# Kernel optimization log

Measured on AMD Instinct MI355X. Metric: run time of the kernel, lower is better.

## Reference

```python
import jax, jax.numpy as jnp
import numpy as np

TAU = 0.2  # temperature from __init__
EPS = 1e-12  # F.normalize eps


def setup_inputs() -> dict:
    key = jax.random.key(0)
    k1, k2, k3 = jax.random.split(key, 3)
    N, D = 131072, 1024
    return {
        "query": jax.random.normal(k1, (D,), dtype=jnp.float32),
        "K": jax.random.normal(k2, (N, D), dtype=jnp.float32),
        "V": jax.random.normal(k3, (N, D), dtype=jnp.float32),
        "topk": 32,
    }


def reference(query, K, V, topk):
    # q = F.normalize(query, dim=-1)
    q = query / jnp.maximum(jnp.linalg.norm(query, axis=-1, keepdims=True), EPS)
    # logits: [N] cosine-sim / tau (K rows are assumed pre-normalized by write())
    logits = (K @ q) / TAU
    # top-k branch (N > topk)
    vals, idxs = jax.lax.top_k(logits, topk)          # [topk], [topk]
    attn = jax.nn.softmax(vals, axis=-1)              # [topk]
    out = attn @ V[idxs]                              # [D]
    full_attn = jnp.zeros_like(logits).at[idxs].set(attn)  # [N]
    return out, full_attn
```

## Files before the change

### kernel.cpp

```cpp
#include <hip/hip_runtime.h>
#include <float.h>
#include <math.h>

#define DIM    1024
#define NROWS  131072
#define TOPK   32
#define TAU    0.2f
#define CHUNK  512
#define NCHUNK (NROWS / CHUNK)
#define NCAND  (NCHUNK * TOPK)

__global__ __launch_bounds__(256) void logits_kernel(const float* __restrict__ Km,
                                                     const float* __restrict__ q,
                                                     float* __restrict__ logits,
                                                     float* __restrict__ full_attn) {
    __shared__ float q_s[DIM];
    const int t = threadIdx.x;
    *reinterpret_cast<float4*>(q_s + t * 4) =
        *reinterpret_cast<const float4*>(q + t * 4);
    __syncthreads();

    const int lane = t & 63;
    const int wave = t >> 6;
    const int sub  = lane & 15;
    const int rsel = lane >> 4;
    const int row  = (blockIdx.x * 4 + wave) * 4 + rsel;

    const float* kr = Km + (size_t)row * DIM;
    float acc = 0.f;
    #pragma unroll
    for (int c = 0; c < 16; ++c) {
        const int fo = c * 64 + sub * 4;
        float4 kv = *reinterpret_cast<const float4*>(kr + fo);
        float4 qv = *reinterpret_cast<const float4*>(q_s + fo);
        acc = fmaf(kv.x, qv.x, acc);
        acc = fmaf(kv.y, qv.y, acc);
        acc = fmaf(kv.z, qv.z, acc);
        acc = fmaf(kv.w, qv.w, acc);
    }
    #pragma unroll
    for (int off = 1; off < 16; off <<= 1) acc += __shfl_xor(acc, off, 64);

    if (sub == 0) {
        logits[row]    = acc;
        full_attn[row] = 0.f;
    }
}

__global__ __launch_bounds__(64) void topk_local_kernel(const float* __restrict__ logits,
                                                        float* __restrict__ cand_val,
                                                        int* __restrict__ cand_idx) {
    const int lane = threadIdx.x;
    const int base = blockIdx.x * CHUNK;

    float v[8]; int gi[8];
    float4 a = *reinterpret_cast<const float4*>(logits + base + lane * 4);
    float4 b = *reinterpret_cast<const float4*>(logits + base + 256 + lane * 4);
    v[0] = a.x; v[1] = a.y; v[2] = a.z; v[3] = a.w;
    v[4] = b.x; v[5] = b.y; v[6] = b.z; v[7] = b.w;
    #pragma unroll
    for (int j = 0; j < 4; ++j) gi[j] = base + lane * 4 + j;
    #pragma unroll
    for (int j = 0; j < 4; ++j) gi[4 + j] = base + 256 + lane * 4 + j;

    for (int r = 0; r < TOPK; ++r) {
        float m = v[0]; int mi = gi[0];
        #pragma unroll
        for (int j = 1; j < 8; ++j)
            if (v[j] > m || (v[j] == m && gi[j] < mi)) { m = v[j]; mi = gi[j]; }
        #pragma unroll
        for (int off = 32; off > 0; off >>= 1) {
            float ov = __shfl_xor(m, off, 64);
            int   oi = __shfl_xor(mi, off, 64);
            if (ov > m || (ov == m && oi < mi)) { m = ov; mi = oi; }
        }
        #pragma unroll
        for (int j = 0; j < 8; ++j)
            if (gi[j] == mi) v[j] = -FLT_MAX;
        if (lane == 0) {
            cand_val[blockIdx.x * TOPK + r] = m;
            cand_idx[blockIdx.x * TOPK + r] = mi;
        }
    }
}

__global__ __launch_bounds__(256) void final_kernel(const float* __restrict__ cand_val,
                                                    const int* __restrict__ cand_idx,
                                                    const float* __restrict__ q,
                                                    const float* __restrict__ Vm,
                                                    float* __restrict__ out,
                                                    float* __restrict__ full_attn) {
    const int t = threadIdx.x;
    const int lane = t & 63, wave = t >> 6;
    __shared__ float wred_v[4];
    __shared__ int   wred_i[4];
    __shared__ float tval[TOPK];
    __shared__ int   tidx[TOPK];
    __shared__ float attn_s[TOPK];
    __shared__ float red4[4];
    __shared__ float scale_s;

    float ss = 0.f;
    for (int i = t; i < DIM; i += 256) { float vq = q[i]; ss = fmaf(vq, vq, ss); }
    #pragma unroll
    for (int off = 32; off > 0; off >>= 1) ss += __shfl_xor(ss, off, 64);
    if (lane == 0) red4[wave] = ss;
    __syncthreads();
    if (t == 0) {
        float s = red4[0] + red4[1] + red4[2] + red4[3];
        scale_s = 1.0f / (fmaxf(sqrtf(s), 1e-12f) * TAU);
    }

    float v[32]; int gi[32];
    #pragma unroll
    for (int k = 0; k < 32; ++k) {
        int c = t + 256 * k;
        v[k]  = cand_val[c];
        gi[k] = cand_idx[c];
    }
    float m = v[0]; int mi = gi[0];
    #pragma unroll
    for (int k = 1; k < 32; ++k)
        if (v[k] > m || (v[k] == m && gi[k] < mi)) { m = v[k]; mi = gi[k]; }

    __syncthreads();

    for (int r = 0; r < TOPK; ++r) {
        float wm = m; int wmi = mi;
        #pragma unroll
        for (int off = 32; off > 0; off >>= 1) {
            float ov = __shfl_xor(wm, off, 64);
            int   oi = __shfl_xor(wmi, off, 64);
            if (ov > wm || (ov == wm && oi < wmi)) { wm = ov; wmi = oi; }
        }
        if (lane == 0) { wred_v[wave] = wm; wred_i[wave] = wmi; }
        __syncthreads();
        float gm = wred_v[0]; int gmi = wred_i[0];
        #pragma unroll
        for (int w = 1; w < 4; ++w) {
            float ov = wred_v[w]; int oi = wred_i[w];
            if (ov > gm || (ov == gm && oi < gmi)) { gm = ov; gmi = oi; }
        }
        if (t == 0) { tval[r] = gm; tidx[r] = gmi; }
        if (mi == gmi) {
            #pragma unroll
            for (int k = 0; k < 32; ++k)
                if (gi[k] == gmi) v[k] = -FLT_MAX;
            m = v[0]; mi = gi[0];
            #pragma unroll
            for (int k = 1; k < 32; ++k)
                if (v[k] > m || (v[k] == m && gi[k] < mi)) { m = v[k]; mi = gi[k]; }
        }
        __syncthreads();
    }

    const float scale = scale_s;
    float sum = 0.f;
    #pragma unroll
    for (int j = 0; j < TOPK; ++j) sum += expf((tval[j] - tval[0]) * scale);
    if (t < TOPK) attn_s[t] = expf((tval[t] - tval[0]) * scale) / sum;
    __syncthreads();

    if (t < TOPK) full_attn[tidx[t]] = attn_s[t];

    for (int d = t; d < DIM; d += 256) {
        float acc = 0.f;
        #pragma unroll
        for (int j = 0; j < TOPK; ++j)
            acc = fmaf(attn_s[j], Vm[(size_t)tidx[j] * DIM + d], acc);
        out[d] = acc;
    }
}

extern "C" void kernel_launch(void* const* d_in, const int* in_sizes, int n_in,
                              void* d_out, int out_size, void* d_ws, size_t ws_size,
                              hipStream_t stream) {
    const float* q  = (const float*)d_in[0];
    const float* Km = (const float*)d_in[1];
    const float* Vm = (const float*)d_in[2];

    float* out       = (float*)d_out;
    float* full_attn = out + DIM;

    float* logits   = (float*)d_ws;
    float* cand_val = logits + NROWS;
    int*   cand_idx = (int*)(cand_val + NCAND);

    logits_kernel<<<NROWS / 16, 256, 0, stream>>>(Km, q, logits, full_attn);
    topk_local_kernel<<<NCHUNK, 64, 0, stream>>>(logits, cand_val, cand_idx);
    final_kernel<<<1, 256, 0, stream>>>(cand_val, cand_idx, q, Vm, out, full_attn);
}
```

Before: 202.2 us.

## Make logits kernel persistent per wave with register-cached query and double-buffered K loads

The logits kernel now runs 2048 blocks, and each wave processes 16 rows, two at a time with 32 lanes per row. The query is held in registers instead of shared memory, and K rows are software-pipelined with a two-stage register double buffer so the next loads are issued before the current FMAs. This is meant to raise memory-level parallelism and remove the LDS staging and barrier on this bandwidth-bound 512 MB read. In exchange it uses more registers, which can lower occupancy.

```diff
diff --git a/kernel.cpp b/kernel.cpp
--- a/kernel.cpp
+++ b/kernel.cpp
@@ -10,40 +10,61 @@
 #define NCHUNK (NROWS / CHUNK)
 #define NCAND  (NCHUNK * TOPK)
 
+#define LOG_BLOCKS 2048
+#define ROWS_PER_WAVE 16
+#define NITER 8
+
 __global__ __launch_bounds__(256) void logits_kernel(const float* __restrict__ Km,
                                                      const float* __restrict__ q,
                                                      float* __restrict__ logits,
                                                      float* __restrict__ full_attn) {
-    __shared__ float q_s[DIM];
-    const int t = threadIdx.x;
-    *reinterpret_cast<float4*>(q_s + t * 4) =
-        *reinterpret_cast<const float4*>(q + t * 4);
-    __syncthreads();
-
+    const int t    = threadIdx.x;
     const int lane = t & 63;
     const int wave = t >> 6;
-    const int sub  = lane & 15;
-    const int rsel = lane >> 4;
-    const int row  = (blockIdx.x * 4 + wave) * 4 + rsel;
-
-    const float* kr = Km + (size_t)row * DIM;
-    float acc = 0.f;
-    #pragma unroll
-    for (int c = 0; c < 16; ++c) {
-        const int fo = c * 64 + sub * 4;
-        float4 kv = *reinterpret_cast<const float4*>(kr + fo);
-        float4 qv = *reinterpret_cast<const float4*>(q_s + fo);
-        acc = fmaf(kv.x, qv.x, acc);
-        acc = fmaf(kv.y, qv.y, acc);
-        acc = fmaf(kv.z, qv.z, acc);
-        acc = fmaf(kv.w, qv.w, acc);
-    }
-    #pragma unroll
-    for (int off = 1; off < 16; off <<= 1) acc += __shfl_xor(acc, off, 64);
-
-    if (sub == 0) {
-        logits[row]    = acc;
-        full_attn[row] = 0.f;
+    const int sub  = lane & 31;
+    const int rsel = lane >> 5;
+
+    float4 qv[8];
+    #pragma unroll
+    for (int p = 0; p < 8; ++p)
+        qv[p] = *reinterpret_cast<const float4*>(q + p * 128 + sub * 4);
+
+    const int gwave = blockIdx.x * 4 + wave;
+    const int rbase = gwave * ROWS_PER_WAVE;
+    const float* kptr = Km + (size_t)(rbase + rsel) * DIM + sub * 4;
+
+    float4 buf[2][8];
+    #pragma unroll
+    for (int p = 0; p < 8; ++p)
+        buf[0][p] = *reinterpret_cast<const float4*>(kptr + p * 128);
+
+    #pragma unroll
+    for (int r = 0; r < NITER; ++r) {
+        const float* knext = kptr + 2 * DIM;
+        if (r < NITER - 1) {
+            #pragma unroll
+            for (int p = 0; p < 8; ++p)
+                buf[(r + 1) & 1][p] = *reinterpret_cast<const float4*>(knext + p * 128);
+        }
+        float a0 = 0.f, a1 = 0.f, a2 = 0.f, a3 = 0.f;
+        #pragma unroll
+        for (int p = 0; p < 8; ++p) {
+            float4 kv = buf[r & 1][p];
+            float4 qq = qv[p];
+            a0 = fmaf(kv.x, qq.x, a0);
+            a1 = fmaf(kv.y, qq.y, a1);
+            a2 = fmaf(kv.z, qq.z, a2);
+            a3 = fmaf(kv.w, qq.w, a3);
+        }
+        float acc = (a0 + a1) + (a2 + a3);
+        #pragma unroll
+        for (int off = 1; off < 32; off <<= 1) acc += __shfl_xor(acc, off, 64);
+        if (sub == 0) {
+            const int row = rbase + 2 * r + rsel;
+            logits[row]    = acc;
+            full_attn[row] = 0.f;
+        }
+        kptr = knext;
     }
 }
 
@@ -186,7 +207,7 @@
     float* cand_val = logits + NROWS;
     int*   cand_idx = (int*)(cand_val + NCAND);
 
-    logits_kernel<<<NROWS / 16, 256, 0, stream>>>(Km, q, logits, full_attn);
+    logits_kernel<<<LOG_BLOCKS, 256, 0, stream>>>(Km, q, logits, full_attn);
     topk_local_kernel<<<NCHUNK, 64, 0, stream>>>(logits, cand_val, cand_idx);
     final_kernel<<<1, 256, 0, stream>>>(cand_val, cand_idx, q, Vm, out, full_attn);
 }
```

New measurement: 207.4 us. 1.03x slower.
